# Optimization experiments

Measured on AMD Instinct MI355X. Metric: run time of the kernel, lower is better.

The kernel has to match this reference:

```python
import jax, jax.numpy as jnp
import numpy as np

N, L, H, Q = 64, 258, 1024, 256
WINDOW = 16.0
DEV_POW = 128.0  # 2 * (window/2)^2, Luong local-p sigma = D/2


def setup_inputs() -> dict:
    key = jax.random.key(0)
    k1, k2, k3, k4, k5, k6 = jax.random.split(key, 6)
    encoder_outputs = jax.random.normal(k1, (N, L, H), dtype=jnp.float32)
    decoder_h_t = jax.random.normal(k2, (N, Q, H), dtype=jnp.float32)
    src_len = jax.random.randint(k3, (N,), 32, L + 1).astype(jnp.int32)
    # window centers within each source sentence
    p_t = jax.random.uniform(k4, (N,), dtype=jnp.float32) * (src_len.astype(jnp.float32) - 1.0)
    W_a = jax.random.normal(k5, (H, H), dtype=jnp.float32) * (1.0 / np.sqrt(H))
    W_c = jax.random.normal(k6, (H, 2 * H), dtype=jnp.float32) * (1.0 / np.sqrt(2 * H))
    return {"encoder_outputs": encoder_outputs, "decoder_h_t": decoder_h_t,
            "src_len": src_len, "p_t": p_t, "W_a": W_a, "W_c": W_c}


def reference(encoder_outputs, decoder_h_t, src_len, p_t, W_a, W_c):
    n, l, h = encoder_outputs.shape
    idx = jnp.arange(l, dtype=jnp.float32)  # index_matrix, length == max_length == L

    # local_p window: [p_t - D, p_t + D], clamped to [0, src_len]
    src_end = src_len.astype(jnp.float32)
    attn_start = jnp.maximum(p_t - WINDOW, 0.0)          # [N]
    attn_end = jnp.minimum(p_t + WINDOW, src_end)        # [N]
    mask = (idx[None, :] < attn_start[:, None]) | (idx[None, :] > attn_end[:, None])  # [N,L]

    # Luong 'general' score: h_t^T W_a h_s -> [N,Q,L]
    score = jnp.einsum('nqh,hk,nlk->nql', decoder_h_t, W_a, encoder_outputs)

    score = jnp.where(mask[:, None, :], -1e9, score)
    align = jax.nn.softmax(score, axis=2)                 # [N,Q,L]

    # gaussian reweighting centered at p_t
    gauss = jnp.exp(-((idx[None, :] - p_t[:, None]) ** 2) / DEV_POW)  # [N,L]
    align = align * gauss[:, None, :]

    context = jnp.einsum('nql,nlh->nqh', align, encoder_outputs)      # [N,Q,H]
    cat = jnp.concatenate([context, decoder_h_t], axis=2)             # [N,Q,2H]
    return jnp.tanh(cat @ W_c.T)                                      # [N,Q,H]
```

## Files before the change

### kernel.cpp

```cpp
#include <hip/hip_runtime.h>
#include <hip/hip_bf16.h>
#include <cstdint>

#define DEVINL __device__ __forceinline__

typedef __attribute__((ext_vector_type(8))) short short8;
typedef __attribute__((ext_vector_type(4))) float f32x4;
typedef __attribute__((ext_vector_type(4))) unsigned short u16x4;

static constexpr int NB = 64, LL = 258, HH = 1024, QQ = 256;
static constexpr int WROWS = 33;
static constexpr int MU = 2176;
static constexpr int VTN = 4096;

static constexpr size_t OFF_META = 0;
static constexpr size_t SZ_WE   = (size_t)MU * HH * 2;
static constexpr size_t OFF_WEHI = 1024;
static constexpr size_t OFF_WELO = OFF_WEHI + SZ_WE;
static constexpr size_t OFF_WAHI = OFF_WELO + SZ_WE;
static constexpr size_t OFF_WALO = OFF_WAHI + (size_t)HH * HH * 2;
static constexpr size_t OFF_WCBF = OFF_WALO + (size_t)HH * HH * 2;
static constexpr size_t OFF_HBF  = OFF_WCBF + (size_t)HH * 2 * HH * 2;
static constexpr size_t OFF_U    = OFF_HBF + (size_t)NB * QQ * HH * 2;
static constexpr size_t OFF_UHI  = OFF_U;
static constexpr size_t OFF_ULO  = OFF_U + (size_t)MU * HH * 2;
static constexpr size_t OFF_CTX  = OFF_U + (size_t)MU * HH * 4;
static constexpr size_t OFF_VT   = OFF_CTX + (size_t)NB * QQ * HH * 2;

DEVINL unsigned short f2bf(float x) {
    union { float f; uint32_t u; } v; v.f = x;
    uint32_t u = v.u;
    uint32_t r = (u + 0x7FFFu + ((u >> 16) & 1u)) >> 16;
    return (unsigned short)r;
}
DEVINL float bf2f(unsigned short b) {
    union { uint32_t u; float f; } v; v.u = ((uint32_t)b) << 16;
    return v.f;
}

template <typename T>
DEVINL void lds_load16(const T* g, T* l) {
    __builtin_amdgcn_global_load_lds(
        (const __attribute__((address_space(1))) void*)g,
        (__attribute__((address_space(3))) void*)l, 16, 0, 0);
}

DEVINL float fast_tanh(float x) {
    float e = __expf(2.0f * x);
    return 1.0f - 2.0f / (e + 1.0f);
}

DEVINL void window_of(float p, int sl, int& ls, int& lc) {
    float se = (float)sl;
    float s = fmaxf(p - 16.0f, 0.0f);
    float e = fminf(p + 16.0f, se);
    ls = (int)ceilf(s);
    int le = (int)floorf(e); if (le > LL - 1) le = LL - 1;
    lc = le - ls + 1;
    if (lc < 0) lc = 0;
    if (lc > WROWS) lc = WROWS;
}

__global__ __launch_bounds__(256) void k_prep(const float* __restrict__ enc,
                                              const float* __restrict__ ht,
                                              const float* __restrict__ pt,
                                              const int* __restrict__ slen,
                                              const float* __restrict__ Wa,
                                              const float* __restrict__ Wc,
                                              unsigned short* __restrict__ wehi,
                                              unsigned short* __restrict__ welo,
                                              unsigned short* __restrict__ wahi,
                                              unsigned short* __restrict__ walo,
                                              unsigned short* __restrict__ wcbf,
                                              unsigned short* __restrict__ hbf) {
    const int b = blockIdx.x, t = threadIdx.x;
    if (b < MU) {
        int r = b;
        const float* src = nullptr;
        bool valid = false;
        if (r < NB * WROWS) {
            int n = r / WROWS, li = r - n * WROWS;
            int ls, lc;
            window_of(pt[n], slen[n], ls, lc);
            if (li < lc) { valid = true; src = enc + ((size_t)n * LL + ls + li) * HH; }
        }
        f32x4 v;
        if (valid) v = ((const f32x4*)src)[t];
        else { v[0] = 0.f; v[1] = 0.f; v[2] = 0.f; v[3] = 0.f; }
        u16x4 h, l;
#pragma unroll
        for (int j = 0; j < 4; ++j) {
            unsigned short hb = f2bf(v[j]);
            h[j] = hb;
            l[j] = f2bf(v[j] - bf2f(hb));
        }
        size_t o = (size_t)r * HH / 4 + t;
        ((u16x4*)wehi)[o] = h;
        ((u16x4*)welo)[o] = l;
    } else if (b < MU + 1024) {
        int i = (b - MU) * 256 + t;
        f32x4 v = ((const f32x4*)Wa)[i];
        u16x4 h, l;
#pragma unroll
        for (int j = 0; j < 4; ++j) {
            unsigned short hb = f2bf(v[j]);
            h[j] = hb;
            l[j] = f2bf(v[j] - bf2f(hb));
        }
        ((u16x4*)wahi)[i] = h;
        ((u16x4*)walo)[i] = l;
    } else if (b < MU + 1024 + 2048) {
        int i = (b - MU - 1024) * 256 + t;
        f32x4 v = ((const f32x4*)Wc)[i];
        u16x4 h;
#pragma unroll
        for (int j = 0; j < 4; ++j) h[j] = f2bf(v[j]);
        ((u16x4*)wcbf)[i] = h;
    } else {
        int i = (b - MU - 3072) * 256 + t;
        f32x4 v = ((const f32x4*)ht)[i];
        u16x4 h;
#pragma unroll
        for (int j = 0; j < 4; ++j) h[j] = f2bf(v[j]);
        ((u16x4*)hbf)[i] = h;
    }
}

__global__ __launch_bounds__(256) void k_ugemm64(const unsigned short* __restrict__ Ahi,
                                                 const unsigned short* __restrict__ Alo,
                                                 const unsigned short* __restrict__ Bhi,
                                                 const unsigned short* __restrict__ Blo,
                                                 unsigned short* __restrict__ Uhi,
                                                 unsigned short* __restrict__ Ulo) {
    __shared__ unsigned short sAh[2][64 * 32], sAl[2][64 * 32], sBh[2][64 * 32], sBl[2][64 * 32];
    const int tid = threadIdx.x;
    const int w = tid >> 6, lane = tid & 63;
    const int m0 = blockIdx.y * 64, n0 = blockIdx.x * 64;
    const int wr = w >> 1, wc = w & 1;
    const int r16 = lane & 15, khalf = lane >> 4;
    const int srow = tid >> 2;
    const int scol = ((tid & 3) ^ ((tid >> 3) & 3)) * 8;
    const int ldso = tid * 8;
    const int kslot = (khalf ^ ((r16 >> 1) & 3)) * 8;
    f32x4 acc[2][2] = {};

    auto stage = [&](int buf, int kb) {
        lds_load16(Ahi + (size_t)(m0 + srow) * HH + kb + scol, &sAh[buf][ldso]);
        lds_load16(Alo + (size_t)(m0 + srow) * HH + kb + scol, &sAl[buf][ldso]);
        lds_load16(Bhi + (size_t)(n0 + srow) * HH + kb + scol, &sBh[buf][ldso]);
        lds_load16(Blo + (size_t)(n0 + srow) * HH + kb + scol, &sBl[buf][ldso]);
    };

    stage(0, 0);
    for (int t = 0; t < 32; ++t) {
        const int buf = t & 1;
        asm volatile("s_waitcnt vmcnt(0)" ::: "memory");
        __builtin_amdgcn_s_barrier();
        short8 ah[2], al[2], bh[2], bl[2];
#pragma unroll
        for (int f = 0; f < 2; ++f) {
            int ai = (wr * 32 + f * 16 + r16) * 32 + kslot;
            ah[f] = *(const short8*)&sAh[buf][ai];
            al[f] = *(const short8*)&sAl[buf][ai];
            int bi = (wc * 32 + f * 16 + r16) * 32 + kslot;
            bh[f] = *(const short8*)&sBh[buf][bi];
            bl[f] = *(const short8*)&sBl[buf][bi];
        }
        if (t + 1 < 32) stage(buf ^ 1, (t + 1) * 32);
        asm volatile("s_waitcnt lgkmcnt(0)" ::: "memory");
        __builtin_amdgcn_sched_barrier(0);
#pragma unroll
        for (int mf = 0; mf < 2; ++mf)
#pragma unroll
            for (int nf = 0; nf < 2; ++nf) {
                acc[mf][nf] = __builtin_amdgcn_mfma_f32_16x16x32_bf16(ah[mf], bh[nf], acc[mf][nf], 0, 0, 0);
                acc[mf][nf] = __builtin_amdgcn_mfma_f32_16x16x32_bf16(ah[mf], bl[nf], acc[mf][nf], 0, 0, 0);
                acc[mf][nf] = __builtin_amdgcn_mfma_f32_16x16x32_bf16(al[mf], bh[nf], acc[mf][nf], 0, 0, 0);
            }
        __builtin_amdgcn_s_barrier();
    }
    const int rg = lane >> 4;
#pragma unroll
    for (int mf = 0; mf < 2; ++mf)
#pragma unroll
        for (int nf = 0; nf < 2; ++nf)
#pragma unroll
            for (int r = 0; r < 4; ++r) {
                int m = m0 + wr * 32 + mf * 16 + rg * 4 + r;
                int nn = n0 + wc * 32 + nf * 16 + r16;
                float v = acc[mf][nf][r];
                unsigned short h = f2bf(v);
                Uhi[(size_t)m * HH + nn] = h;
                Ulo[(size_t)m * HH + nn] = f2bf(v - bf2f(h));
            }
}

__global__ __launch_bounds__(256) void k_vgemm64(const unsigned short* __restrict__ Wc1,
                                                 const unsigned short* __restrict__ Bhi,
                                                 const unsigned short* __restrict__ Blo,
                                                 unsigned short* __restrict__ VT) {
    __shared__ unsigned short sA[2][64 * 32], sBh[2][64 * 32], sBl[2][64 * 32];
    const int tid = threadIdx.x;
    const int w = tid >> 6, lane = tid & 63;
    const int m0 = blockIdx.y * 64, n0 = blockIdx.x * 64;
    const int wr = w >> 1, wc = w & 1;
    const int r16 = lane & 15, khalf = lane >> 4;
    const int srow = tid >> 2;
    const int scol = ((tid & 3) ^ ((tid >> 3) & 3)) * 8;
    const int ldso = tid * 8;
    const int kslot = (khalf ^ ((r16 >> 1) & 3)) * 8;
    f32x4 acc[2][2] = {};

    auto stage = [&](int buf, int kb) {
        lds_load16(Wc1 + (size_t)(m0 + srow) * (2 * HH) + kb + scol, &sA[buf][ldso]);
        lds_load16(Bhi + (size_t)(n0 + srow) * HH + kb + scol, &sBh[buf][ldso]);
        lds_load16(Blo + (size_t)(n0 + srow) * HH + kb + scol, &sBl[buf][ldso]);
    };

    stage(0, 0);
    for (int t = 0; t < 32; ++t) {
        const int buf = t & 1;
        asm volatile("s_waitcnt vmcnt(0)" ::: "memory");
        __builtin_amdgcn_s_barrier();
        short8 af[2], bh[2], bl[2];
#pragma unroll
        for (int f = 0; f < 2; ++f) {
            af[f] = *(const short8*)&sA[buf][(wr * 32 + f * 16 + r16) * 32 + kslot];
            int bi = (wc * 32 + f * 16 + r16) * 32 + kslot;
            bh[f] = *(const short8*)&sBh[buf][bi];
            bl[f] = *(const short8*)&sBl[buf][bi];
        }
        if (t + 1 < 32) stage(buf ^ 1, (t + 1) * 32);
        asm volatile("s_waitcnt lgkmcnt(0)" ::: "memory");
        __builtin_amdgcn_sched_barrier(0);
#pragma unroll
        for (int mf = 0; mf < 2; ++mf)
#pragma unroll
            for (int nf = 0; nf < 2; ++nf) {
                acc[mf][nf] = __builtin_amdgcn_mfma_f32_16x16x32_bf16(af[mf], bh[nf], acc[mf][nf], 0, 0, 0);
                acc[mf][nf] = __builtin_amdgcn_mfma_f32_16x16x32_bf16(af[mf], bl[nf], acc[mf][nf], 0, 0, 0);
            }
        __builtin_amdgcn_s_barrier();
    }
    const int rg = lane >> 4;
#pragma unroll
    for (int mf = 0; mf < 2; ++mf)
#pragma unroll
        for (int nf = 0; nf < 2; ++nf)
#pragma unroll
            for (int r = 0; r < 4; ++r) {
                int o = m0 + wr * 32 + mf * 16 + rg * 4 + r;
                int wrow = n0 + wc * 32 + nf * 16 + r16;
                int n = wrow / WROWS, li = wrow - n * WROWS;
                if (n < NB)
                    VT[(size_t)o * VTN + n * 64 + li] = f2bf(acc[mf][nf][r]);
            }
}

__global__ __launch_bounds__(256) void k_attn2(const float* __restrict__ ht,
                                               const unsigned short* __restrict__ Uhi,
                                               const unsigned short* __restrict__ Ulo,
                                               const unsigned short* __restrict__ VT,
                                               const float* __restrict__ pt,
                                               const int* __restrict__ slen,
                                               unsigned short* __restrict__ ctxP) {
    __shared__ float sPart[4][32 * 48];
    __shared__ float sScore[32 * 48];
    __shared__ unsigned short sPhi[32 * 72];
    __shared__ unsigned short sPlo[32 * 72];

    const int tid = threadIdx.x;
    const int w = tid >> 6, lane = tid & 63;
    const int n = blockIdx.x >> 3, q0 = (blockIdx.x & 7) * 32;
    int ls, lc;
    window_of(pt[n], slen[n], ls, lc);
    const float p = pt[n];
    const int r16 = lane & 15, khalf = lane >> 4, rg = lane >> 4;

    const float* hbase = ht + ((size_t)(n * QQ + q0)) * HH;
    const unsigned short* uhbase = Uhi + (size_t)n * WROWS * HH;
    const unsigned short* ulbase = Ulo + (size_t)n * WROWS * HH;

    f32x4 acc[2][3] = {};
    for (int ks = 0; ks < 8; ++ks) {
        int kcol = w * 256 + ks * 32 + khalf * 8;
        short8 ah[2], al[2];
#pragma unroll
        for (int mf = 0; mf < 2; ++mf) {
            const float* src = hbase + (size_t)(mf * 16 + r16) * HH + kcol;
            f32x4 v0 = *(const f32x4*)src;
            f32x4 v1 = *(const f32x4*)(src + 4);
            float vv[8] = {v0[0], v0[1], v0[2], v0[3], v1[0], v1[1], v1[2], v1[3]};
#pragma unroll
            for (int j = 0; j < 8; ++j) {
                unsigned short hb = f2bf(vv[j]);
                ah[mf][j] = (short)hb;
                al[mf][j] = (short)f2bf(vv[j] - bf2f(hb));
            }
        }
#pragma unroll
        for (int nf = 0; nf < 3; ++nf) {
            size_t uoff = (size_t)(nf * 16 + r16) * HH + kcol;
            short8 bh = *(const short8*)(uhbase + uoff);
            short8 bl = *(const short8*)(ulbase + uoff);
#pragma unroll
            for (int mf = 0; mf < 2; ++mf) {
                acc[mf][nf] = __builtin_amdgcn_mfma_f32_16x16x32_bf16(ah[mf], bh, acc[mf][nf], 0, 0, 0);
                acc[mf][nf] = __builtin_amdgcn_mfma_f32_16x16x32_bf16(ah[mf], bl, acc[mf][nf], 0, 0, 0);
                acc[mf][nf] = __builtin_amdgcn_mfma_f32_16x16x32_bf16(al[mf], bh, acc[mf][nf], 0, 0, 0);
            }
        }
    }
#pragma unroll
    for (int mf = 0; mf < 2; ++mf)
#pragma unroll
        for (int nf = 0; nf < 3; ++nf)
#pragma unroll
            for (int r = 0; r < 4; ++r)
                sPart[w][(mf * 16 + rg * 4 + r) * 48 + nf * 16 + r16] = acc[mf][nf][r];
    __syncthreads();

    {
        int q = tid >> 3, g = tid & 7;
        float sc6[6];
#pragma unroll
        for (int s = 0; s < 6; ++s) {
            int li = g + 8 * s;
            int o = q * 48 + li;
            sc6[s] = sPart[0][o] + sPart[1][o] + sPart[2][o] + sPart[3][o];
        }
        float mx = -1e30f;
#pragma unroll
        for (int s = 0; s < 6; ++s) { int li = g + 8 * s; if (li < lc) mx = fmaxf(mx, sc6[s]); }
        for (int off = 1; off < 8; off <<= 1) mx = fmaxf(mx, __shfl_xor(mx, off, 8));
        float sum = 0.f, ex[6];
#pragma unroll
        for (int s = 0; s < 6; ++s) {
            int li = g + 8 * s;
            float e = (li < lc) ? __expf(sc6[s] - mx) : 0.f;
            ex[s] = e; sum += e;
        }
        for (int off = 1; off < 8; off <<= 1) sum += __shfl_xor(sum, off, 8);
        float inv = 1.0f / sum;
#pragma unroll
        for (int s = 0; s < 6; ++s) {
            int li = g + 8 * s;
            float d = (float)(ls + li) - p;
            float gs = __expf(-(d * d) * (1.0f / 128.0f));
            sScore[q * 48 + li] = ex[s] * inv * gs;
        }
    }
    __syncthreads();

    {
        int row = tid >> 3, c0 = (tid & 7) * 8;
#pragma unroll
        for (int j = 0; j < 8; ++j) {
            int c = c0 + j;
            float pv = (c < 48) ? sScore[row * 48 + c] : 0.f;
            unsigned short hb = f2bf(pv);
            sPhi[row * 72 + c] = hb;
            sPlo[row * 72 + c] = f2bf(pv - bf2f(hb));
        }
    }
    __syncthreads();

    short8 pa[2][2], plq[2][2];
#pragma unroll
    for (int mf = 0; mf < 2; ++mf)
#pragma unroll
        for (int ks = 0; ks < 2; ++ks) {
            pa[mf][ks]  = *(const short8*)&sPhi[(mf * 16 + r16) * 72 + ks * 32 + khalf * 8];
            plq[mf][ks] = *(const short8*)&sPlo[(mf * 16 + r16) * 72 + ks * 32 + khalf * 8];
        }
    const unsigned short* vtb = VT + n * 64 + khalf * 8;
    const size_t tile16 = (size_t)(n * 4 + w) * 16;
#pragma unroll
    for (int half = 0; half < 2; ++half) {
        f32x4 accB[2][8] = {};
        const int hcol0 = w * 256 + half * 128;
#pragma unroll
        for (int nf = 0; nf < 8; ++nf) {
            const int o = hcol0 + nf * 16 + r16;
#pragma unroll
            for (int ks = 0; ks < 2; ++ks) {
                short8 bfrag = *(const short8*)(vtb + (size_t)o * VTN + ks * 32);
#pragma unroll
                for (int mf = 0; mf < 2; ++mf) {
                    accB[mf][nf] = __builtin_amdgcn_mfma_f32_16x16x32_bf16(pa[mf][ks], bfrag, accB[mf][nf], 0, 0, 0);
                    accB[mf][nf] = __builtin_amdgcn_mfma_f32_16x16x32_bf16(plq[mf][ks], bfrag, accB[mf][nf], 0, 0, 0);
                }
            }
        }
#pragma unroll
        for (int mf = 0; mf < 2; ++mf) {
            const int br = q0 + mf * 16;
            const int m  = (br >> 7) * 4 + ((br >> 4) & 3);
            const int wr2 = (br >> 6) & 1;
            const int ib = m * 2 + half;
#pragma unroll
            for (int nfp = 0; nfp < 4; ++nfp) {
                short8 pk;
#pragma unroll
                for (int r = 0; r < 4; ++r) {
                    pk[r]     = (short)f2bf(accB[mf][2 * nfp][r]);
                    pk[4 + r] = (short)f2bf(accB[mf][2 * nfp + 1][r]);
                }
                const int tid_o = wr2 * 256 + nfp * 64 + lane;
                size_t off = (((tile16 + ib) * 512) + tid_o) * 8;
                *(short8*)&ctxP[off] = pk;
            }
        }
    }
}

#define RD_A(dst, buf, mh, mq, ksub) \
    dst = *(const short8*)&sA[(buf) * 16384 + (mh) * 8192 + \
        (wr * 64 + (mq) * 16 + r16) * 64 + ((((ksub) * 4 + kg) ^ (r16 & 7)) * 8)];
#define RD_B(dst, buf, nh, nq, ksub) \
    dst = *(const short8*)&sB[(buf) * 16384 + (nh) * 8192 + \
        (wc * 32 + (nq) * 16 + r16) * 64 + ((((ksub) * 4 + kg) ^ (r16 & 7)) * 8)];
#define MFMA_QUAD(MH, NH) \
    _Pragma("unroll") \
    for (int mq = 0; mq < 4; ++mq) { \
        _Pragma("unroll") \
        for (int nq = 0; nq < 2; ++nq) { \
            f32x4 c = acc[(MH) * 4 + mq][(NH) * 2 + nq]; \
            c = __builtin_amdgcn_mfma_f32_16x16x32_bf16(a[mq][0], b[nq][0], c, 0, 0, 0); \
            c = __builtin_amdgcn_mfma_f32_16x16x32_bf16(a[mq][1], b[nq][1], c, 0, 0, 0); \
            acc[(MH) * 4 + mq][(NH) * 2 + nq] = c; \
        } \
    }
#define PHASE_SYNC() \
    __builtin_amdgcn_s_barrier(); \
    asm volatile("s_waitcnt lgkmcnt(0)" ::: "memory"); \
    __builtin_amdgcn_sched_barrier(0);

__global__ __launch_bounds__(512, 1) void k_out_gemm256(
    const unsigned short* __restrict__ Ahf,
    const unsigned short* __restrict__ Bt,
    const unsigned short* __restrict__ Cp,
    float* __restrict__ out) {
    extern __shared__ unsigned short lds[];
    unsigned short* sA = lds;
    unsigned short* sB = lds + 32768;

    const int tid = threadIdx.x;
    const int wid = tid >> 6, lane = tid & 63;
    const int bid = blockIdx.x;
    const int swz = (bid & 7) * 32 + (bid >> 3);
    const int mt = swz >> 2, ntile = swz & 3;
    const int m0 = mt * 256, n0 = ntile * 256;
    const int wr = wid >> 2, wc = wid & 3;
    const int r16 = lane & 15, kg = lane >> 4;

    const int srow = lane >> 3;
    const int kswz = ((lane & 7) ^ srow) * 8;

    f32x4 acc[8][4] = {};

    auto stage_tile = [&](int buf, int kb) {
#pragma unroll
        for (int half = 0; half < 2; ++half) {
#pragma unroll
            for (int i = 0; i < 2; ++i) {
                int r = half * 128 + i * 64 + wid * 8 + srow;
                lds_load16(Ahf + (size_t)(m0 + r) * HH + kb + kswz,
                           sA + buf * 16384 + half * 8192 + i * 4096 + wid * 512);
            }
#pragma unroll
            for (int i = 0; i < 2; ++i) {
                int r = half * 128 + i * 64 + wid * 8 + srow;
                lds_load16(Bt + (size_t)(n0 + r) * (2 * HH) + 1024 + kb + kswz,
                           sB + buf * 16384 + half * 8192 + i * 4096 + wid * 512);
            }
        }
    };

    stage_tile(0, 0);
    asm volatile("s_waitcnt vmcnt(4)" ::: "memory");
    __builtin_amdgcn_s_barrier();

    short8 a[4][2], b[2][2];
    for (int t = 0; t < 16; ++t) {
        const int buf = t & 1;
#pragma unroll
        for (int mq = 0; mq < 4; ++mq) { RD_A(a[mq][0], buf, 0, mq, 0) RD_A(a[mq][1], buf, 0, mq, 1) }
#pragma unroll
        for (int nq = 0; nq < 2; ++nq) { RD_B(b[nq][0], buf, 0, nq, 0) RD_B(b[nq][1], buf, 0, nq, 1) }
        if (t + 1 < 16) stage_tile(buf ^ 1, (t + 1) * 64);
        PHASE_SYNC()
        __builtin_amdgcn_s_setprio(1);
        MFMA_QUAD(0, 0)
        __builtin_amdgcn_s_setprio(0);
        if (t + 1 < 16) { asm volatile("s_waitcnt vmcnt(8)" ::: "memory"); }
        else            { asm volatile("s_waitcnt vmcnt(0)" ::: "memory"); }
        __builtin_amdgcn_s_barrier();
#pragma unroll
        for (int nq = 0; nq < 2; ++nq) { RD_B(b[nq][0], buf, 1, nq, 0) RD_B(b[nq][1], buf, 1, nq, 1) }
        PHASE_SYNC()
        __builtin_amdgcn_s_setprio(1);
        MFMA_QUAD(0, 1)
        __builtin_amdgcn_s_setprio(0);
        __builtin_amdgcn_s_barrier();
#pragma unroll
        for (int mq = 0; mq < 4; ++mq) { RD_A(a[mq][0], buf, 1, mq, 0) RD_A(a[mq][1], buf, 1, mq, 1) }
        PHASE_SYNC()
        __builtin_amdgcn_s_setprio(1);
        MFMA_QUAD(1, 1)
        __builtin_amdgcn_s_setprio(0);
        __builtin_amdgcn_s_barrier();
#pragma unroll
        for (int nq = 0; nq < 2; ++nq) { RD_B(b[nq][0], buf, 0, nq, 0) RD_B(b[nq][1], buf, 0, nq, 1) }
        PHASE_SYNC()
        __builtin_amdgcn_s_setprio(1);
        MFMA_QUAD(1, 0)
        __builtin_amdgcn_s_setprio(0);
        asm volatile("s_waitcnt vmcnt(4)" ::: "memory");
        __builtin_amdgcn_s_barrier();
    }

    const unsigned short* cbase = Cp + (((size_t)(mt * 4 + ntile)) * 16) * 512 * 8;
    short8 cv[16];
#pragma unroll
    for (int ib = 0; ib < 16; ++ib)
        cv[ib] = *(const short8*)&cbase[((size_t)ib * 512 + tid) * 8];
#pragma unroll
    for (int m = 0; m < 8; ++m)
#pragma unroll
        for (int n = 0; n < 4; ++n) {
            int row = m0 + (m >> 2) * 128 + wr * 64 + (m & 3) * 16 + kg * 4;
            int col = n0 + (n >> 1) * 128 + wc * 32 + (n & 1) * 16 + r16;
            const int ib = m * 2 + (n >> 1);
#pragma unroll
            for (int r = 0; r < 4; ++r) {
                float cadd = bf2f((unsigned short)cv[ib][(n & 1) * 4 + r]);
                out[(size_t)(row + r) * HH + col] = fast_tanh(acc[m][n][r] + cadd);
            }
        }
}

extern "C" void kernel_launch(void* const* d_in, const int* in_sizes, int n_in,
                              void* d_out, int out_size, void* d_ws, size_t ws_size,
                              hipStream_t stream) {
    const float* enc  = (const float*)d_in[0];
    const float* ht   = (const float*)d_in[1];
    const int*   slen = (const int*)d_in[2];
    const float* pt   = (const float*)d_in[3];
    const float* Wa   = (const float*)d_in[4];
    const float* Wc   = (const float*)d_in[5];
    float* out = (float*)d_out;

    char* ws = (char*)d_ws;
    unsigned short* wehi = (unsigned short*)(ws + OFF_WEHI);
    unsigned short* welo = (unsigned short*)(ws + OFF_WELO);
    unsigned short* wahi = (unsigned short*)(ws + OFF_WAHI);
    unsigned short* walo = (unsigned short*)(ws + OFF_WALO);
    unsigned short* wcbf = (unsigned short*)(ws + OFF_WCBF);
    unsigned short* hbf  = (unsigned short*)(ws + OFF_HBF);
    unsigned short* uhi  = (unsigned short*)(ws + OFF_UHI);
    unsigned short* ulo  = (unsigned short*)(ws + OFF_ULO);
    unsigned short* ctxP = (unsigned short*)(ws + OFF_CTX);
    unsigned short* vt   = (unsigned short*)(ws + OFF_VT);

    hipFuncSetAttribute((const void*)k_out_gemm256,
                        hipFuncAttributeMaxDynamicSharedMemorySize, 131072);

    hipLaunchKernelGGL(k_prep, dim3(MU + 1024 + 2048 + 16384), dim3(256), 0, stream,
                       enc, ht, pt, slen, Wa, Wc, wehi, welo, wahi, walo, wcbf, hbf);
    hipLaunchKernelGGL(k_ugemm64, dim3(HH / 64, MU / 64), dim3(256), 0, stream,
                       wehi, welo, wahi, walo, uhi, ulo);
    hipLaunchKernelGGL(k_vgemm64, dim3(MU / 64, HH / 64), dim3(256), 0, stream,
                       wcbf, wehi, welo, vt);
    hipLaunchKernelGGL(k_attn2, dim3(NB * 8), dim3(256), 0, stream,
                       ht, uhi, ulo, vt, pt, slen, ctxP);
    hipLaunchKernelGGL(k_out_gemm256, dim3(256), dim3(512), 131072, stream,
                       hbf, wcbf, ctxP, out);
}
```

Before: 158.4 us.

## Replace 256x256 pipelined output GEMM with simple 128x128 tile kernel

Replaces the 512-thread, 256x256-tile, double-buffered, phase-scheduled output GEMM with a 256-thread 128x128-tile kernel. The new kernel uses static LDS, single-buffers with a full wait, and launches 1024 blocks instead of 256. The attention kernel's context write layout is changed to match the new tile and wave mapping. This gives more blocks and higher occupancy across CUs, but gives up load/compute overlap and adds redundant global traffic from the smaller tiles.

```diff
diff --git a/kernel.cpp b/kernel.cpp
--- a/kernel.cpp
+++ b/kernel.cpp
@@ -374,7 +374,6 @@
             plq[mf][ks] = *(const short8*)&sPlo[(mf * 16 + r16) * 72 + ks * 32 + khalf * 8];
         }
     const unsigned short* vtb = VT + n * 64 + khalf * 8;
-    const size_t tile16 = (size_t)(n * 4 + w) * 16;
 #pragma unroll
     for (int half = 0; half < 2; ++half) {
         f32x4 accB[2][8] = {};
@@ -392,150 +391,103 @@
                 }
             }
         }
+        const int nt = w * 2 + half;
 #pragma unroll
         for (int mf = 0; mf < 2; ++mf) {
-            const int br = q0 + mf * 16;
-            const int m  = (br >> 7) * 4 + ((br >> 4) & 3);
-            const int wr2 = (br >> 6) & 1;
-            const int ib = m * 2 + half;
-#pragma unroll
-            for (int nfp = 0; nfp < 4; ++nfp) {
+            const int rb = q0 + mf * 16;
+            const int mt = n * 2 + (rb >> 7);
+            const int rowbit = (rb >> 6) & 1;
+            const int mq = (rb >> 4) & 3;
+#pragma unroll
+            for (int pp = 0; pp < 4; ++pp) {
                 short8 pk;
 #pragma unroll
                 for (int r = 0; r < 4; ++r) {
-                    pk[r]     = (short)f2bf(accB[mf][2 * nfp][r]);
-                    pk[4 + r] = (short)f2bf(accB[mf][2 * nfp + 1][r]);
+                    pk[r]     = (short)f2bf(accB[mf][2 * pp][r]);
+                    pk[4 + r] = (short)f2bf(accB[mf][2 * pp + 1][r]);
                 }
-                const int tid_o = wr2 * 256 + nfp * 64 + lane;
-                size_t off = (((tile16 + ib) * 512) + tid_o) * 8;
+                const int widc = rowbit * 2 + (pp >> 1);
+                const int fid = mq * 2 + (pp & 1);
+                size_t off = ((((size_t)(mt * 8 + nt) * 4 + widc) * 8 + fid) * 64 + lane) * 8;
                 *(short8*)&ctxP[off] = pk;
             }
         }
     }
 }
 
-#define RD_A(dst, buf, mh, mq, ksub) \
-    dst = *(const short8*)&sA[(buf) * 16384 + (mh) * 8192 + \
-        (wr * 64 + (mq) * 16 + r16) * 64 + ((((ksub) * 4 + kg) ^ (r16 & 7)) * 8)];
-#define RD_B(dst, buf, nh, nq, ksub) \
-    dst = *(const short8*)&sB[(buf) * 16384 + (nh) * 8192 + \
-        (wc * 32 + (nq) * 16 + r16) * 64 + ((((ksub) * 4 + kg) ^ (r16 & 7)) * 8)];
-#define MFMA_QUAD(MH, NH) \
-    _Pragma("unroll") \
-    for (int mq = 0; mq < 4; ++mq) { \
-        _Pragma("unroll") \
-        for (int nq = 0; nq < 2; ++nq) { \
-            f32x4 c = acc[(MH) * 4 + mq][(NH) * 2 + nq]; \
-            c = __builtin_amdgcn_mfma_f32_16x16x32_bf16(a[mq][0], b[nq][0], c, 0, 0, 0); \
-            c = __builtin_amdgcn_mfma_f32_16x16x32_bf16(a[mq][1], b[nq][1], c, 0, 0, 0); \
-            acc[(MH) * 4 + mq][(NH) * 2 + nq] = c; \
-        } \
-    }
-#define PHASE_SYNC() \
-    __builtin_amdgcn_s_barrier(); \
-    asm volatile("s_waitcnt lgkmcnt(0)" ::: "memory"); \
-    __builtin_amdgcn_sched_barrier(0);
-
-__global__ __launch_bounds__(512, 1) void k_out_gemm256(
+__global__ __launch_bounds__(256) void k_out_gemm128(
     const unsigned short* __restrict__ Ahf,
     const unsigned short* __restrict__ Bt,
     const unsigned short* __restrict__ Cp,
     float* __restrict__ out) {
-    extern __shared__ unsigned short lds[];
-    unsigned short* sA = lds;
-    unsigned short* sB = lds + 32768;
+    __shared__ unsigned short sA[128 * 64], sB[128 * 64];
 
     const int tid = threadIdx.x;
     const int wid = tid >> 6, lane = tid & 63;
     const int bid = blockIdx.x;
-    const int swz = (bid & 7) * 32 + (bid >> 3);
-    const int mt = swz >> 2, ntile = swz & 3;
-    const int m0 = mt * 256, n0 = ntile * 256;
-    const int wr = wid >> 2, wc = wid & 3;
+    const int swz = (bid & 7) * 128 + (bid >> 3);
+    const int mt = swz >> 3, nt = swz & 7;
+    const int m0 = mt * 128, n0 = nt * 128;
+    const int wr = wid >> 1, wc = wid & 1;
     const int r16 = lane & 15, kg = lane >> 4;
 
-    const int srow = lane >> 3;
-    const int kswz = ((lane & 7) ^ srow) * 8;
-
-    f32x4 acc[8][4] = {};
-
-    auto stage_tile = [&](int buf, int kb) {
-#pragma unroll
-        for (int half = 0; half < 2; ++half) {
-#pragma unroll
-            for (int i = 0; i < 2; ++i) {
-                int r = half * 128 + i * 64 + wid * 8 + srow;
-                lds_load16(Ahf + (size_t)(m0 + r) * HH + kb + kswz,
-                           sA + buf * 16384 + half * 8192 + i * 4096 + wid * 512);
-            }
-#pragma unroll
-            for (int i = 0; i < 2; ++i) {
-                int r = half * 128 + i * 64 + wid * 8 + srow;
-                lds_load16(Bt + (size_t)(n0 + r) * (2 * HH) + 1024 + kb + kswz,
-                           sB + buf * 16384 + half * 8192 + i * 4096 + wid * 512);
-            }
-        }
-    };
-
-    stage_tile(0, 0);
-    asm volatile("s_waitcnt vmcnt(4)" ::: "memory");
-    __builtin_amdgcn_s_barrier();
-
-    short8 a[4][2], b[2][2];
+    const int srow8 = lane >> 3;
+    const int kswz = ((lane & 7) ^ srow8) * 8;
+
+    f32x4 acc[4][4] = {};
+
     for (int t = 0; t < 16; ++t) {
-        const int buf = t & 1;
-#pragma unroll
-        for (int mq = 0; mq < 4; ++mq) { RD_A(a[mq][0], buf, 0, mq, 0) RD_A(a[mq][1], buf, 0, mq, 1) }
-#pragma unroll
-        for (int nq = 0; nq < 2; ++nq) { RD_B(b[nq][0], buf, 0, nq, 0) RD_B(b[nq][1], buf, 0, nq, 1) }
-        if (t + 1 < 16) stage_tile(buf ^ 1, (t + 1) * 64);
-        PHASE_SYNC()
-        __builtin_amdgcn_s_setprio(1);
-        MFMA_QUAD(0, 0)
-        __builtin_amdgcn_s_setprio(0);
-        if (t + 1 < 16) { asm volatile("s_waitcnt vmcnt(8)" ::: "memory"); }
-        else            { asm volatile("s_waitcnt vmcnt(0)" ::: "memory"); }
-        __builtin_amdgcn_s_barrier();
-#pragma unroll
-        for (int nq = 0; nq < 2; ++nq) { RD_B(b[nq][0], buf, 1, nq, 0) RD_B(b[nq][1], buf, 1, nq, 1) }
-        PHASE_SYNC()
-        __builtin_amdgcn_s_setprio(1);
-        MFMA_QUAD(0, 1)
-        __builtin_amdgcn_s_setprio(0);
-        __builtin_amdgcn_s_barrier();
-#pragma unroll
-        for (int mq = 0; mq < 4; ++mq) { RD_A(a[mq][0], buf, 1, mq, 0) RD_A(a[mq][1], buf, 1, mq, 1) }
-        PHASE_SYNC()
-        __builtin_amdgcn_s_setprio(1);
-        MFMA_QUAD(1, 1)
-        __builtin_amdgcn_s_setprio(0);
-        __builtin_amdgcn_s_barrier();
-#pragma unroll
-        for (int nq = 0; nq < 2; ++nq) { RD_B(b[nq][0], buf, 0, nq, 0) RD_B(b[nq][1], buf, 0, nq, 1) }
-        PHASE_SYNC()
-        __builtin_amdgcn_s_setprio(1);
-        MFMA_QUAD(1, 0)
-        __builtin_amdgcn_s_setprio(0);
-        asm volatile("s_waitcnt vmcnt(4)" ::: "memory");
-        __builtin_amdgcn_s_barrier();
-    }
-
-    const unsigned short* cbase = Cp + (((size_t)(mt * 4 + ntile)) * 16) * 512 * 8;
-    short8 cv[16];
-#pragma unroll
-    for (int ib = 0; ib < 16; ++ib)
-        cv[ib] = *(const short8*)&cbase[((size_t)ib * 512 + tid) * 8];
-#pragma unroll
-    for (int m = 0; m < 8; ++m)
-#pragma unroll
-        for (int n = 0; n < 4; ++n) {
-            int row = m0 + (m >> 2) * 128 + wr * 64 + (m & 3) * 16 + kg * 4;
-            int col = n0 + (n >> 1) * 128 + wc * 32 + (n & 1) * 16 + r16;
-            const int ib = m * 2 + (n >> 1);
+        const int kb = t * 64;
+        if (t > 0) __syncthreads();
+#pragma unroll
+        for (int i = 0; i < 4; ++i) {
+            int row = i * 32 + wid * 8 + srow8;
+            lds_load16(Ahf + (size_t)(m0 + row) * HH + kb + kswz,
+                       &sA[i * 2048 + wid * 512]);
+            lds_load16(Bt + (size_t)(n0 + row) * (2 * HH) + 1024 + kb + kswz,
+                       &sB[i * 2048 + wid * 512]);
+        }
+        asm volatile("s_waitcnt vmcnt(0)" ::: "memory");
+        __syncthreads();
+
+        short8 a[4][2];
+#pragma unroll
+        for (int mq = 0; mq < 4; ++mq)
+#pragma unroll
+            for (int ks = 0; ks < 2; ++ks)
+                a[mq][ks] = *(const short8*)&sA[(wr * 64 + mq * 16 + r16) * 64 +
+                                                (((ks * 4 + kg) ^ (r16 & 7)) * 8)];
+#pragma unroll
+        for (int nq = 0; nq < 4; ++nq) {
+            short8 b0 = *(const short8*)&sB[(wc * 64 + nq * 16 + r16) * 64 +
+                                            (((0 + kg) ^ (r16 & 7)) * 8)];
+            short8 b1 = *(const short8*)&sB[(wc * 64 + nq * 16 + r16) * 64 +
+                                            (((4 + kg) ^ (r16 & 7)) * 8)];
+#pragma unroll
+            for (int mq = 0; mq < 4; ++mq) {
+                acc[mq][nq] = __builtin_amdgcn_mfma_f32_16x16x32_bf16(a[mq][0], b0, acc[mq][nq], 0, 0, 0);
+                acc[mq][nq] = __builtin_amdgcn_mfma_f32_16x16x32_bf16(a[mq][1], b1, acc[mq][nq], 0, 0, 0);
+            }
+        }
+    }
+
+    const size_t cbase = (((size_t)(mt * 8 + nt) * 4 + wid) * 8) * 512 + (size_t)lane * 8;
+    short8 cv[8];
+#pragma unroll
+    for (int f = 0; f < 8; ++f)
+        cv[f] = *(const short8*)&Cp[cbase + (size_t)f * 512];
+#pragma unroll
+    for (int mq = 0; mq < 4; ++mq)
+#pragma unroll
+        for (int nq = 0; nq < 4; ++nq) {
+            const int f = mq * 2 + (nq >> 1);
+            const int part = (nq & 1) * 4;
+            int row = m0 + wr * 64 + mq * 16 + kg * 4;
+            int col = n0 + wc * 64 + nq * 16 + r16;
 #pragma unroll
             for (int r = 0; r < 4; ++r) {
-                float cadd = bf2f((unsigned short)cv[ib][(n & 1) * 4 + r]);
-                out[(size_t)(row + r) * HH + col] = fast_tanh(acc[m][n][r] + cadd);
+                float cadd = bf2f((unsigned short)cv[f][part + r]);
+                out[(size_t)(row + r) * HH + col] = fast_tanh(acc[mq][nq][r] + cadd);
             }
         }
 }
@@ -563,9 +515,6 @@
     unsigned short* ctxP = (unsigned short*)(ws + OFF_CTX);
     unsigned short* vt   = (unsigned short*)(ws + OFF_VT);
 
-    hipFuncSetAttribute((const void*)k_out_gemm256,
-                        hipFuncAttributeMaxDynamicSharedMemorySize, 131072);
-
     hipLaunchKernelGGL(k_prep, dim3(MU + 1024 + 2048 + 16384), dim3(256), 0, stream,
                        enc, ht, pt, slen, Wa, Wc, wehi, welo, wahi, walo, wcbf, hbf);
     hipLaunchKernelGGL(k_ugemm64, dim3(HH / 64, MU / 64), dim3(256), 0, stream,
@@ -574,6 +523,6 @@
                        wcbf, wehi, welo, vt);
     hipLaunchKernelGGL(k_attn2, dim3(NB * 8), dim3(256), 0, stream,
                        ht, uhi, ulo, vt, pt, slen, ctxP);
-    hipLaunchKernelGGL(k_out_gemm256, dim3(256), dim3(512), 131072, stream,
+    hipLaunchKernelGGL(k_out_gemm128, dim3(1024), dim3(256), 0, stream,
                        hbf, wcbf, ctxP, out);
 }
```

Result: no change. 158.7 us (+0.2%).
